# Kernel tuning notes

Hardware: AMD Instinct MI355X
Metric: run time of the kernel (lower is better)

Reference implementation:

```python
import jax, jax.numpy as jnp
import numpy as np
from jax import lax

D = 386      # model dim
H = 8        # heads
DH = 64      # dim per head
FF = 4 * D   # 1544, ff inner dim
FUSED = H * DH + DH + DH + 2 * FF  # 3728 fused proj width
S = 200      # patch_len


def setup_inputs() -> dict:
    key = jax.random.key(0)
    ks = iter(jax.random.split(key, 64))
    nrm = lambda shape, s=0.02: jax.random.normal(next(ks), shape, jnp.float32) * s
    inp = {"input": jax.random.normal(next(ks), (4, 2 * S, 3, 40, 40), jnp.float32)}
    inp["conv_w"] = nrm((D, 3, 3, 3), 0.1)
    inp["conv_b"] = jnp.zeros((D,), jnp.float32)
    inp["cls_token"] = nrm((D,), 1.0)
    for pre in ("uni", "mm"):
        inp[f"{pre}_ln"] = jnp.ones((4, D), jnp.float32)
        inp[f"{pre}_fused"] = nrm((4, D, FUSED))
        inp[f"{pre}_attn_out"] = nrm((4, H * DH, D))
        inp[f"{pre}_ff_out"] = nrm((4, FF, D))
    inp["ca_ln"] = jnp.ones((4, D), jnp.float32)
    inp["ca_q"] = nrm((4, D, H * DH))
    inp["ca_kv"] = nrm((4, D, 2 * DH))
    inp["ca_out"] = nrm((4, H * DH, D))
    inp["ca_ff1"] = nrm((4, D, 2 * FF))
    inp["ca_ff2"] = nrm((4, FF, D))
    inp["logit_ln"] = jnp.ones((D,), jnp.float32)
    inp["logit_w"] = nrm((D, 2))
    return inp


def layer_norm(x, g, eps=1e-5):
    m = x.mean(-1, keepdims=True)
    v = ((x - m) ** 2).mean(-1, keepdims=True)
    return (x - m) * lax.rsqrt(v + eps) * g


def rotate_half(t):
    t1, t2 = jnp.split(t, 2, axis=-1)
    return jnp.concatenate([-t2, t1], axis=-1)


def rotary_pos(n, d):
    inv = 1.0 / (10000.0 ** (jnp.arange(0, d, 2, dtype=jnp.float32) / d))
    fr = jnp.arange(n, dtype=jnp.float32)[:, None] * inv[None, :]
    return jnp.concatenate([fr, fr], axis=-1)  # [n, d]


def ptb(x, g, wf, wo, wff):
    # ParallelTransformerBlock (no residual): multi-query attn + parallel SwiGLU ff
    b, n, _ = x.shape
    xn = layer_norm(x, g)
    f = xn @ wf  # [b,n,FUSED]
    q = f[..., : H * DH].reshape(b, n, H, DH).transpose(0, 2, 1, 3)  # [b,h,n,d]
    k = f[..., H * DH : H * DH + DH]          # [b,n,d] single-head
    v = f[..., H * DH + DH : H * DH + 2 * DH]  # [b,n,d]
    ff = f[..., H * DH + 2 * DH :]
    pos = rotary_pos(n, DH)
    c, s = jnp.cos(pos), jnp.sin(pos)
    q = q * c + rotate_half(q) * s
    k = k * c + rotate_half(k) * s
    q = q * (DH ** -0.5)
    sim = jnp.einsum('bhid,bjd->bhij', q, k)
    mask = jnp.triu(jnp.ones((n, n), bool), 1)
    sim = jnp.where(mask, -jnp.finfo(sim.dtype).max, sim)
    attn = jax.nn.softmax(sim, axis=-1)
    out = jnp.einsum('bhij,bjd->bhid', attn, v).transpose(0, 2, 1, 3).reshape(b, n, H * DH)
    x1, gate = jnp.split(ff, 2, axis=-1)
    return out @ wo + (jax.nn.silu(gate) * x1) @ wff


def cross_attn(x, ctx, g, wq, wkv, wo, wf1, wf2):
    # CrossAttention with parallel_ff=True (context not normed)
    b, n, _ = x.shape
    xn = layer_norm(x, g)
    q = (xn @ wq).reshape(b, n, H, DH).transpose(0, 2, 1, 3) * (DH ** -0.5)
    k, v = jnp.split(ctx @ wkv, 2, axis=-1)  # [b,m,d] each, single-head
    sim = jnp.einsum('bhid,bjd->bhij', q, k)
    attn = jax.nn.softmax(sim, axis=-1)
    out = jnp.einsum('bhij,bjd->bhid', attn, v).transpose(0, 2, 1, 3).reshape(b, n, H * DH) @ wo
    h1, gate = jnp.split(xn @ wf1, 2, axis=-1)
    return out + (jax.nn.silu(gate) * h1) @ wf2


def reference(input, conv_w, conv_b, cls_token, uni_ln, uni_fused, uni_attn_out, uni_ff_out,
              mm_ln, mm_fused, mm_attn_out, mm_ff_out, ca_ln, ca_q, ca_kv, ca_out,
              ca_ff1, ca_ff2, logit_ln, logit_w):
    b = input.shape[0]

    def embed(img):  # [b,S,3,40,40] -> [b,S+1,D]
        x = img.reshape(b * S, 3, 40, 40)
        x = lax.conv_general_dilated(x, conv_w, (2, 2), 'VALID',
                                     dimension_numbers=('NCHW', 'OIHW', 'NCHW'))
        x = jax.nn.relu(x + conv_b[None, :, None, None])
        x = x.mean(axis=(2, 3)).reshape(b, S, D)  # adaptive avg pool (1,1)
        cls = jnp.broadcast_to(cls_token, (b, 1, D))
        return jnp.concatenate([x, cls], axis=1)

    # original forward uses embed_abnormal for BOTH chunks
    a = embed(input[:, :S])
    nrm = embed(input[:, S:])
    for i in range(4):
        a = a + ptb(a, uni_ln[i], uni_fused[i], uni_attn_out[i], uni_ff_out[i])
        nrm = nrm + ptb(nrm, uni_ln[i], uni_fused[i], uni_attn_out[i], uni_ff_out[i])
    for i in range(4):
        a = a + ptb(a, mm_ln[i], mm_fused[i], mm_attn_out[i], mm_ff_out[i])
        a = a + cross_attn(a, nrm, ca_ln[i], ca_q[i], ca_kv[i], ca_out[i], ca_ff1[i], ca_ff2[i])
    cls = a[:, -1]
    return layer_norm(cls, logit_ln) @ logit_w
```

## Files before the change

kernel.cpp:

```cpp
#include <hip/hip_runtime.h>
#include <hip/hip_bf16.h>
#include <math.h>

#define Dm 386
#define Hh 8
#define DHd 64
#define FFf 1544
#define FUS 3728
#define STOK 200
#define NTOK 201

typedef __attribute__((ext_vector_type(8))) short bf16x8;
typedef __attribute__((ext_vector_type(4))) float f32x4;

__device__ inline void gload16(const void* g, void* lds) {
  __builtin_amdgcn_global_load_lds((const __attribute__((address_space(1))) void*)g,
                                   (__attribute__((address_space(3))) void*)lds, 16, 0, 0);
}

__device__ inline short bfb(float v) {
  union { float f; unsigned u; } c; c.f = v;
  unsigned r = (c.u + 0x7fff + ((c.u >> 16) & 1)) >> 16;
  if ((c.u & 0x7f800000) == 0x7f800000) r = c.u >> 16;
  return (short)r;
}

__device__ inline void stage_coords(int lane, int& sr, int& sg) {
  int o = lane * 16;
  int rhi = (o >> 7) & 7;
  int r2 = (o >> 8) & 1;
  int r0 = ((o >> 6) & 1) ^ r2;
  sr = (rhi << 1) | r0;
  sg = ((o >> 4) & 3) ^ (sr & 3);
}

__global__ void misc_prep_kernel(const float* __restrict__ cw, __hip_bfloat16* __restrict__ wt,
                                 float* __restrict__ ct, float* __restrict__ st,
                                 const float* __restrict__ cls, float* __restrict__ act) {
  int b = blockIdx.x, t = threadIdx.x;
  if (b < 50) {
    int idx = b * 256 + t;
    if (idx < 400 * 32) {
      int n = idx >> 5, k = idx & 31;
      float v = (n < Dm && k < 27) ? cw[n * 27 + k] : 0.f;
      wt[idx] = __float2bfloat16(v);
    }
  } else if (b < 76) {
    int idx = (b - 50) * 256 + t;
    if (idx < 208 * 32) {
      int i = idx >> 5, d = idx & 31;
      float inv = exp2f((float)d * -0.41524101186f);
      float a = (float)i * inv;
      ct[idx] = cosf(a);
      st[idx] = sinf(a);
    }
  } else {
    int idx = (b - 76) * 256 + t;
    if (idx < 8 * Dm) {
      int r = idx / Dm, d = idx - r * Dm;
      act[((size_t)r * NTOK + STOK) * Dm + d] = cls[d];
    }
  }
}

struct CvtPack {
  const float* W[11];
  __hip_bfloat16* Bt[11];
};

__device__ void convert_body(int id, float* tile, const CvtPack& p) {
  static const int KK[11]    = {386, 512, 1544, 386, 512, 1544, 386, 386, 512, 386, 1544};
  static const int NN[11]    = {3728, 386, 386, 3728, 386, 386, 512, 128, 386, 3088, 386};
  static const int KPO[11]   = {416, 512, 1568, 416, 512, 1568, 416, 416, 512, 416, 1568};
  static const int KPOUT[11] = {416, 2080, 2080, 416, 2080, 2080, 416, 416, 2080, 416, 2080};
  static const int NTIL[11]  = {30, 4, 4, 30, 4, 4, 4, 1, 4, 25, 4};
  static const int LSTR[11]  = {1597440, 1064960, 1064960, 1597440, 1064960, 1064960,
                                1544192, 53248, 1064960, 1544192, 1064960};
  static const int CNT[11]   = {840, 128, 400, 840, 128, 400, 112, 28, 128, 700, 400};
  int wi = 0;
  while (wi < 10 && id >= CNT[wi]) { id -= CNT[wi]; ++wi; }
  int K = KK[wi], N = NN[wi];
  int ntil = NTIL[wi];
  int kpout = KPOUT[wi];
  int z = id & 3; id >>= 2;
  int kt = id / ntil, bx = id - kt * ntil;
  int k0 = kt * 64, n0 = bx * 128;
  const float* Wl = p.W[wi] + (size_t)z * K * N;
  __hip_bfloat16* Btl = p.Bt[wi] + (size_t)z * LSTR[wi];

  int tid = threadIdx.x;
  bool nfull = (n0 + 128 <= N);

  if (nfull && (N & 3) == 0) {
    int t4 = tid & 31, tk = tid >> 5;
    int nb = n0 + t4 * 4;
    #pragma unroll
    for (int j = 0; j < 4; ++j) {
      int kl = tk + 16 * j;
      int k = k0 + kl;
      float4 v = {0.f, 0.f, 0.f, 0.f};
      if (k < K) v = *(const float4*)(Wl + (size_t)k * N + nb);
      float* tr = tile + kl * 130 + t4 * 4;
      tr[0] = v.x; tr[1] = v.y; tr[2] = v.z; tr[3] = v.w;
    }
  } else {
    int t2 = tid & 63, tk = tid >> 6;
    int nb = n0 + t2 * 2;
    #pragma unroll
    for (int j = 0; j < 8; ++j) {
      int kl = tk + 8 * j;
      int k = k0 + kl;
      float2 v = {0.f, 0.f};
      if (k < K) {
        const float* src = Wl + (size_t)k * N + nb;
        if (nfull) {
          v = *(const float2*)src;
        } else {
          if (nb < N) v.x = src[0];
          if (nb + 1 < N) v.y = src[1];
        }
      }
      tile[kl * 130 + t2 * 2] = v.x;
      tile[kl * 130 + t2 * 2 + 1] = v.y;
    }
  }
  __syncthreads();

  int kv = KPO[wi] - k0; if (kv > 64) kv = 64;
  int tk8 = tid & 7;
  int nr = tid >> 3;
  if (tk8 * 8 < kv) {
    #pragma unroll
    for (int h = 0; h < 2; ++h) {
      int n = nr + 64 * h;
      __hip_bfloat16 out[8] __attribute__((aligned(16)));
      #pragma unroll
      for (int e = 0; e < 8; ++e)
        out[e] = __float2bfloat16(tile[(tk8 * 8 + e) * 130 + n]);
      *(int4*)(Btl + (size_t)(n0 + n) * kpout + k0 + tk8 * 8) = *(const int4*)out;
    }
  }
}

__device__ void conv_body(int img, char* smem,
                          const float* __restrict__ input, const __hip_bfloat16* __restrict__ wt,
                          const float* __restrict__ conv_b, float* __restrict__ act) {
  __hip_bfloat16* patches = (__hip_bfloat16*)smem;
  float* pooled = (float*)smem;
  float* biasS = (float*)(smem + 29440);

  int bi = img / 400, fi = img % 400;
  int srow = (fi < STOK) ? bi : (4 + bi);
  int tok = (fi < STOK) ? fi : (fi - STOK);
  float* dst = act + ((size_t)srow * NTOK + tok) * Dm;

  int tid = threadIdx.x;
  const float* img_base = input + (size_t)img * 4800;
  for (int i = tid; i < 400; i += 512) biasS[i] = (i < Dm) ? -conv_b[i] : 0.f;

  for (int p = tid; p < 368; p += 512) {
    short rowv[32] __attribute__((aligned(16)));
    #pragma unroll
    for (int k = 27; k < 32; ++k) rowv[k] = 0;
    if (p < 361) {
      int oy = p / 19, ox = p - oy * 19;
      const float* bp = img_base + (2 * oy) * 40 + 2 * ox;
      #pragma unroll
      for (int c = 0; c < 3; ++c) {
        #pragma unroll
        for (int ky = 0; ky < 3; ++ky) {
          const float* rp = bp + c * 1600 + ky * 40;
          #pragma unroll
          for (int kx = 0; kx < 3; ++kx)
            rowv[c * 9 + ky * 3 + kx] = bfb(rp[kx]);
        }
      }
    } else {
      #pragma unroll
      for (int k = 0; k < 27; ++k) rowv[k] = 0;
    }
    int4* dv = (int4*)(patches + p * 40);
    const int4* sv = (const int4*)rowv;
    #pragma unroll
    for (int q = 0; q < 4; ++q) dv[q] = sv[q];
  }
  __syncthreads();

  int lane = tid & 63, w = tid >> 6;
  int col = lane & 15, rgrp = lane >> 4;

  bf16x8 af[3];
  #pragma unroll
  for (int t = 0; t < 3; ++t) {
    int m = w * 3 + t;
    int row = (m < 23) ? (m * 16 + col) : 0;
    af[t] = *(const bf16x8*)&patches[row * 40 + rgrp * 8];
  }
  __syncthreads();

  for (int n = 0; n < 25; ++n) {
    bf16x8 bfrag = *(const bf16x8*)&wt[(n * 16 + col) * 32 + rgrp * 8];
    float nb = biasS[n * 16 + col];
    f32x4 a0 = {0.f, 0.f, 0.f, 0.f}, a1 = {0.f, 0.f, 0.f, 0.f};
    a0 = __builtin_amdgcn_mfma_f32_16x16x32_bf16(af[0], bfrag, a0, 0, 0, 0);
    a1 = __builtin_amdgcn_mfma_f32_16x16x32_bf16(af[1], bfrag, a1, 0, 0, 0);
    float psum = 0.f;
    #pragma unroll
    for (int j = 0; j < 4; ++j) psum += fmaxf(a0[j], nb);
    if (w == 7) {
      #pragma unroll
      for (int j = 0; j < 4; ++j) {
        int rr = 352 + rgrp * 4 + j;
        psum += (rr < 361) ? fmaxf(a1[j], nb) : 0.f;
      }
    } else {
      #pragma unroll
      for (int j = 0; j < 4; ++j) psum += fmaxf(a1[j], nb);
      f32x4 a2 = {0.f, 0.f, 0.f, 0.f};
      a2 = __builtin_amdgcn_mfma_f32_16x16x32_bf16(af[2], bfrag, a2, 0, 0, 0);
      #pragma unroll
      for (int j = 0; j < 4; ++j) psum += fmaxf(a2[j], nb);
    }
    psum += __shfl_xor(psum, 16);
    psum += __shfl_xor(psum, 32);
    if (lane < 16) pooled[w * 400 + n * 16 + lane] = psum;
  }
  __syncthreads();
  for (int d = tid; d < Dm; d += 512) {
    float s = 0.f;
    #pragma unroll
    for (int ww = 0; ww < 8; ++ww) s += pooled[ww * 400 + d];
    dst[d] = s * (1.f / 361.f) + conv_b[d];
  }
}

__global__ __launch_bounds__(512) void prep_conv_kernel(
    CvtPack p, const float* __restrict__ input, const __hip_bfloat16* __restrict__ wt,
    const float* __restrict__ conv_b, float* __restrict__ act) {
  __shared__ __align__(16) char smem[33280];
  int bid = blockIdx.x;
  int g = bid / 18, r = bid - g * 18;
  if (r < 5) {
    conv_body(g * 5 + r, smem, input, wt, conv_b, act);
  } else {
    int cid = g * 13 + (r - 5);
    if (cid < 4104) convert_body(cid, (float*)smem, p);
  }
}

__global__ __launch_bounds__(64) void ln_kernel(const float* __restrict__ x,
                                                const float* __restrict__ g,
                                                __hip_bfloat16* __restrict__ y) {
  size_t row = blockIdx.x;
  const float* xr = x + row * Dm;
  __hip_bfloat16* yr = y + row * 416;
  int t = threadIdx.x;
  float v[7];
  float lsum = 0.f, lsq = 0.f;
  #pragma unroll
  for (int j = 0; j < 7; ++j) {
    int c = t + 64 * j;
    float val = (c < Dm) ? xr[c] : 0.f;
    v[j] = val;
    lsum += val;
    lsq += val * val;
  }
  #pragma unroll
  for (int o = 32; o > 0; o >>= 1) { lsum += __shfl_xor(lsum, o); lsq += __shfl_xor(lsq, o); }
  float mean = lsum * (1.f / 386.f);
  float var = lsq * (1.f / 386.f) - mean * mean;
  float inv = rsqrtf(var + 1e-5f);
  #pragma unroll
  for (int j = 0; j < 7; ++j) {
    int c = t + 64 * j;
    if (c < 416) {
      float out = (c < Dm) ? (v[j] - mean) * inv * g[c] : 0.f;
      yr[c] = __float2bfloat16(out);
    }
  }
}

template<bool ACC>
__global__ __launch_bounds__(256) void mfma_mm(
    const __hip_bfloat16* __restrict__ A, const __hip_bfloat16* __restrict__ Bt,
    float* __restrict__ C, int M, int N, int Kp) {
  __shared__ short As[128 * 32];
  __shared__ short Bs[128 * 32];
  int tid = threadIdx.x;
  int lane = tid & 63, w = tid >> 6;
  int wr = w >> 1, wc = w & 1;
  int bm = blockIdx.y * 128, bn = blockIdx.x * 128;
  f32x4 acc[4][4] = {};

  int sr, sg;
  stage_coords(lane, sr, sg);
  const __hip_bfloat16* Abase = A + (size_t)(bm + w * 16 + sr) * Kp + sg * 8;
  const __hip_bfloat16* Bbase = Bt + (size_t)(bn + w * 16 + sr) * Kp + sg * 8;
  short* AsW1 = As + w * 512;
  short* AsW2 = As + 2048 + w * 512;
  short* BsW1 = Bs + w * 512;
  short* BsW2 = Bs + 2048 + w * 512;
  size_t rstep = (size_t)64 * Kp;
  int key = (lane & 7) << 4;
  int kg16 = (lane >> 4) * 16;

  for (int k0 = 0; k0 < Kp; k0 += 32) {
    gload16(Abase + k0, AsW1);
    gload16(Abase + k0 + rstep, AsW2);
    gload16(Bbase + k0, BsW1);
    gload16(Bbase + k0 + rstep, BsW2);
    __syncthreads();
    bf16x8 af[4], bfr[4];
    #pragma unroll
    for (int m = 0; m < 4; ++m) {
      int R = wr * 64 + m * 16 + (lane & 15);
      af[m] = *(const bf16x8*)((const char*)As + ((R * 64 + kg16) ^ key));
    }
    #pragma unroll
    for (int n = 0; n < 4; ++n) {
      int R = wc * 64 + n * 16 + (lane & 15);
      bfr[n] = *(const bf16x8*)((const char*)Bs + ((R * 64 + kg16) ^ key));
    }
    #pragma unroll
    for (int m = 0; m < 4; ++m)
      #pragma unroll
      for (int n = 0; n < 4; ++n)
        acc[m][n] = __builtin_amdgcn_mfma_f32_16x16x32_bf16(af[m], bfr[n], acc[m][n], 0, 0, 0);
    __syncthreads();
  }

  int col = lane & 15, rbase = (lane >> 4) * 4;
  #pragma unroll
  for (int m = 0; m < 4; ++m) {
    #pragma unroll
    for (int n = 0; n < 4; ++n) {
      #pragma unroll
      for (int j = 0; j < 4; ++j) {
        int gr = bm + wr * 64 + m * 16 + rbase + j;
        int gc = bn + wc * 64 + n * 16 + col;
        if (gr < M && gc < N) {
          size_t idx = (size_t)gr * N + gc;
          if (ACC) C[idx] += acc[m][n][j]; else C[idx] = acc[m][n][j];
        }
      }
    }
  }
}

__global__ __launch_bounds__(256) void mfma_mm64(
    const __hip_bfloat16* __restrict__ A, const __hip_bfloat16* __restrict__ Bt,
    float* __restrict__ C, int M, int N, int Kp) {
  __shared__ short As[64 * 32];
  __shared__ short Bs[64 * 32];
  int tid = threadIdx.x;
  int lane = tid & 63, w = tid >> 6;
  int wr = w >> 1, wc = w & 1;
  int bm = blockIdx.y * 64, bn = blockIdx.x * 64;
  f32x4 acc[2][2] = {};

  int sr, sg;
  stage_coords(lane, sr, sg);
  const __hip_bfloat16* Abase = A + (size_t)(bm + w * 16 + sr) * Kp + sg * 8;
  const __hip_bfloat16* Bbase = Bt + (size_t)(bn + w * 16 + sr) * Kp + sg * 8;
  short* AsW = As + w * 512;
  short* BsW = Bs + w * 512;
  int key = (lane & 7) << 4;
  int kg16 = (lane >> 4) * 16;

  for (int k0 = 0; k0 < Kp; k0 += 32) {
    gload16(Abase + k0, AsW);
    gload16(Bbase + k0, BsW);
    __syncthreads();
    bf16x8 af[2], bfr[2];
    #pragma unroll
    for (int m = 0; m < 2; ++m) {
      int R = wr * 32 + m * 16 + (lane & 15);
      af[m] = *(const bf16x8*)((const char*)As + ((R * 64 + kg16) ^ key));
    }
    #pragma unroll
    for (int n = 0; n < 2; ++n) {
      int R = wc * 32 + n * 16 + (lane & 15);
      bfr[n] = *(const bf16x8*)((const char*)Bs + ((R * 64 + kg16) ^ key));
    }
    #pragma unroll
    for (int m = 0; m < 2; ++m)
      #pragma unroll
      for (int n = 0; n < 2; ++n)
        acc[m][n] = __builtin_amdgcn_mfma_f32_16x16x32_bf16(af[m], bfr[n], acc[m][n], 0, 0, 0);
    __syncthreads();
  }

  int col = lane & 15, rbase = (lane >> 4) * 4;
  #pragma unroll
  for (int m = 0; m < 2; ++m) {
    #pragma unroll
    for (int n = 0; n < 2; ++n) {
      #pragma unroll
      for (int j = 0; j < 4; ++j) {
        int gr = bm + wr * 32 + m * 16 + rbase + j;
        int gc = bn + wc * 32 + n * 16 + col;
        if (gr < M && gc < N) C[(size_t)gr * N + gc] = acc[m][n][j];
      }
    }
  }
}

__global__ __launch_bounds__(256) void mfma_mm64a(
    const __hip_bfloat16* __restrict__ A, const __hip_bfloat16* __restrict__ Bt,
    float* __restrict__ C, int M, int N, int Kp, int chunk) {
  int kbeg = blockIdx.z * chunk;
  if (kbeg >= Kp) return;
  int kend = min(Kp, kbeg + chunk);
  __shared__ short As[64 * 32];
  __shared__ short Bs[64 * 32];
  int tid = threadIdx.x;
  int lane = tid & 63, w = tid >> 6;
  int wr = w >> 1, wc = w & 1;
  int bm = blockIdx.y * 64, bn = blockIdx.x * 64;
  f32x4 acc[2][2] = {};

  int sr, sg;
  stage_coords(lane, sr, sg);
  const __hip_bfloat16* Abase = A + (size_t)(bm + w * 16 + sr) * Kp + sg * 8;
  const __hip_bfloat16* Bbase = Bt + (size_t)(bn + w * 16 + sr) * Kp + sg * 8;
  short* AsW = As + w * 512;
  short* BsW = Bs + w * 512;
  int key = (lane & 7) << 4;
  int kg16 = (lane >> 4) * 16;

  for (int k0 = kbeg; k0 < kend; k0 += 32) {
    gload16(Abase + k0, AsW);
    gload16(Bbase + k0, BsW);
    __syncthreads();
    bf16x8 af[2], bfr[2];
    #pragma unroll
    for (int m = 0; m < 2; ++m) {
      int R = wr * 32 + m * 16 + (lane & 15);
      af[m] = *(const bf16x8*)((const char*)As + ((R * 64 + kg16) ^ key));
    }
    #pragma unroll
    for (int n = 0; n < 2; ++n) {
      int R = wc * 32 + n * 16 + (lane & 15);
      bfr[n] = *(const bf16x8*)((const char*)Bs + ((R * 64 + kg16) ^ key));
    }
    #pragma unroll
    for (int m = 0; m < 2; ++m)
      #pragma unroll
      for (int n = 0; n < 2; ++n)
        acc[m][n] = __builtin_amdgcn_mfma_f32_16x16x32_bf16(af[m], bfr[n], acc[m][n], 0, 0, 0);
    __syncthreads();
  }

  int col = lane & 15, rbase = (lane >> 4) * 4;
  #pragma unroll
  for (int m = 0; m < 2; ++m) {
    #pragma unroll
    for (int n = 0; n < 2; ++n) {
      #pragma unroll
      for (int j = 0; j < 4; ++j) {
        int gr = bm + wr * 32 + m * 16 + rbase + j;
        int gc = bn + wc * 32 + n * 16 + col;
        if (gr < M && gc < N) unsafeAtomicAdd(&C[(size_t)gr * N + gc], acc[m][n][j]);
      }
    }
  }
}

__global__ void convert_a_kernel(const float* __restrict__ src, __hip_bfloat16* __restrict__ dst,
                                 int M, int K, int Kp) {
  int chunks = Kp >> 3;
  int idx = blockIdx.x * blockDim.x + threadIdx.x;
  if (idx >= M * chunks) return;
  int r = idx / chunks, ch = idx - r * chunks;
  int c = ch * 8;
  const float* sr = src + (size_t)r * K;
  __hip_bfloat16 out[8] __attribute__((aligned(16)));
  #pragma unroll
  for (int e = 0; e < 8; e += 2) {
    int cc = c + e;
    float2 v = {0.f, 0.f};
    if (cc + 1 < K) v = *(const float2*)(sr + cc);
    else if (cc < K) v.x = sr[cc];
    out[e] = __float2bfloat16(v.x);
    out[e + 1] = __float2bfloat16(v.y);
  }
  *(int4*)(dst + (size_t)r * Kp + c) = *(const int4*)out;
}

__global__ __launch_bounds__(256) void attn_silu_kernel(
    const float* __restrict__ Q, int qstride,
    const float* __restrict__ K, int kstride,
    const float* __restrict__ V, int vstride,
    __hip_bfloat16* __restrict__ O, int ostride,
    int causal, float scale,
    const float* __restrict__ ct, const float* __restrict__ st, int dorope,
    int nb, int rows, int x1off, int gateoff) {
  int nf = 26 * nb;
  int tid = threadIdx.x;

  if ((int)blockIdx.x >= nf) {
    int idx = ((int)blockIdx.x - nf) * 256 + tid;
    if (idx >= rows * 196) return;
    int r = idx / 196, ch = idx - r * 196;
    int c = ch * 8;
    __hip_bfloat16 out[8] __attribute__((aligned(16)));
    if (c < FFf) {
      const float* sr = Q + (size_t)r * qstride;
      float4 xa = *(const float4*)(sr + x1off + c);
      float4 xb = *(const float4*)(sr + x1off + c + 4);
      float4 ga = *(const float4*)(sr + gateoff + c);
      float4 gb = *(const float4*)(sr + gateoff + c + 4);
      float xv[8] = {xa.x, xa.y, xa.z, xa.w, xb.x, xb.y, xb.z, xb.w};
      float gv[8] = {ga.x, ga.y, ga.z, ga.w, gb.x, gb.y, gb.z, gb.w};
      #pragma unroll
      for (int e = 0; e < 8; ++e) {
        float g = gv[e];
        out[e] = __float2bfloat16(g / (1.f + __expf(-g)) * xv[e]);
      }
    } else {
      #pragma unroll
      for (int e = 0; e < 8; ++e) out[e] = __float2bfloat16(0.f);
    }
    *(int4*)(O + 512 + (size_t)r * ostride + c) = *(const int4*)out;
    return;
  }

  __shared__ __align__(16) char smembuf[59392];
  short* Ks  = (short*)smembuf;
  short* Ps  = (short*)smembuf;
  short* VTs = (short*)(smembuf + 29696);

  int bb = blockIdx.x / 26;
  int i0 = (blockIdx.x % 26) * 8;
  int lane = tid & 63, w = tid >> 6;
  const float* Qb = Q + (size_t)bb * NTOK * qstride;
  const float* Kb = K + (size_t)bb * NTOK * kstride;
  const float* Vb = V + (size_t)bb * NTOK * vstride;

  int ntiles = causal ? min(13, (i0 + 7) / 16 + 1) : 13;
  int jstage = ntiles * 16;
  int jm = min(jstage, 201);

  {
    int4 z = {0, 0, 0, 0};
    int4* vt4 = (int4*)VTs;
    for (int idx = tid; idx < 64 * 232 * 2 / 16; idx += 256) vt4[idx] = z;
  }
  __syncthreads();

  for (int jj = tid >> 2; jj < jstage; jj += 64) {
    int q4 = tid & 3;
    int dbase = q4 * 16;
    const float* kro = Kb + (size_t)jj * kstride;
    float selfv[16], partv[16];
    #pragma unroll
    for (int f = 0; f < 4; ++f) {
      float4 kv = {0.f, 0.f, 0.f, 0.f};
      if (jj < 201) kv = ((const float4*)(kro + dbase))[f];
      selfv[f * 4 + 0] = kv.x; selfv[f * 4 + 1] = kv.y;
      selfv[f * 4 + 2] = kv.z; selfv[f * 4 + 3] = kv.w;
    }
    if (dorope && jj < 201) {
      int pbase = dbase ^ 32;
      #pragma unroll
      for (int f = 0; f < 4; ++f) {
        float4 kv = ((const float4*)(kro + pbase))[f];
        partv[f * 4 + 0] = kv.x; partv[f * 4 + 1] = kv.y;
        partv[f * 4 + 2] = kv.z; partv[f * 4 + 3] = kv.w;
      }
      const float* cr = ct + jj * 32 + (dbase & 31);
      const float* sr2 = st + jj * 32 + (dbase & 31);
      #pragma unroll
      for (int e = 0; e < 16; ++e) {
        float c = cr[e], s = sr2[e];
        selfv[e] = (dbase < 32) ? (selfv[e] * c - partv[e] * s)
                                : (selfv[e] * c + partv[e] * s);
      }
    }
    #pragma unroll
    for (int f = 0; f < 4; ++f) {
      short4 b;
      b.x = bfb(selfv[f * 4 + 0]); b.y = bfb(selfv[f * 4 + 1]);
      b.z = bfb(selfv[f * 4 + 2]); b.w = bfb(selfv[f * 4 + 3]);
      int colb = dbase * 2 + f * 8;
      *(short4*)((char*)Ks + (jj * 128 + (colb ^ ((jj & 7) << 4)))) = b;
    }
  }
  for (int jj = tid >> 3; jj < jm; jj += 32) {
    int e8 = (tid & 7) * 8;
    const float4* vr = (const float4*)(Vb + (size_t)jj * vstride + e8);
    float4 v0 = vr[0], v1 = vr[1];
    float vv[8] = {v0.x, v0.y, v0.z, v0.w, v1.x, v1.y, v1.z, v1.w};
    #pragma unroll
    for (int e = 0; e < 8; ++e) VTs[(e8 + e) * 232 + jj] = bfb(vv[e]);
  }

  int r = lane & 15, kg = lane >> 4;
  int rg = w * 16 + r;
  int iq = i0 + (rg >> 3);
  if (iq > 200) iq = 200;
  int h = rg & 7;
  const float* qr = Qb + (size_t)iq * qstride + h * 64 + kg * 8;
  float x1[8], x2[8];
  {
    float4 a0 = ((const float4*)qr)[0];
    float4 a1 = ((const float4*)(qr + 4))[0];
    float4 b0 = ((const float4*)(qr + 32))[0];
    float4 b1 = ((const float4*)(qr + 36))[0];
    x1[0] = a0.x; x1[1] = a0.y; x1[2] = a0.z; x1[3] = a0.w;
    x1[4] = a1.x; x1[5] = a1.y; x1[6] = a1.z; x1[7] = a1.w;
    x2[0] = b0.x; x2[1] = b0.y; x2[2] = b0.z; x2[3] = b0.w;
    x2[4] = b1.x; x2[5] = b1.y; x2[6] = b1.z; x2[7] = b1.w;
  }
  if (dorope) {
    const float* cr = ct + iq * 32 + kg * 8;
    const float* sr2 = st + iq * 32 + kg * 8;
    #pragma unroll
    for (int e = 0; e < 8; ++e) {
      float c = cr[e], s = sr2[e];
      float n1 = x1[e] * c - x2[e] * s;
      float n2 = x2[e] * c + x1[e] * s;
      x1[e] = n1; x2[e] = n2;
    }
  }
  bf16x8 aq[2];
  #pragma unroll
  for (int e = 0; e < 8; ++e) {
    aq[0][e] = bfb(x1[e] * scale);
    aq[1][e] = bfb(x2[e] * scale);
  }
  __syncthreads();

  int key = (lane & 7) << 4;
  f32x4 s[13];
  #pragma unroll
  for (int nt = 0; nt < 13; ++nt) {
    s[nt] = (f32x4){0.f, 0.f, 0.f, 0.f};
    if (nt < ntiles) {
      #pragma unroll
      for (int kt = 0; kt < 2; ++kt) {
        int row = nt * 16 + r;
        bf16x8 bk = *(const bf16x8*)((const char*)Ks + ((row * 128 + kt * 64 + kg * 16) ^ key));
        s[nt] = __builtin_amdgcn_mfma_f32_16x16x32_bf16(aq[kt], bk, s[nt], 0, 0, 0);
      }
    }
  }

  int jcol = lane & 15;
  int ibase[4];
  #pragma unroll
  for (int reg = 0; reg < 4; ++reg) ibase[reg] = i0 + ((w * 16 + kg * 4 + reg) >> 3);

  f32x4 mx = {-1e30f, -1e30f, -1e30f, -1e30f};
  #pragma unroll
  for (int nt = 0; nt < 13; ++nt) {
    if (nt >= ntiles) continue;
    int j = nt * 16 + jcol;
    #pragma unroll
    for (int reg = 0; reg < 4; ++reg) {
      bool ok = (j <= 200) && (!causal || j <= ibase[reg]);
      float sv = ok ? s[nt][reg] : -1e30f;
      s[nt][reg] = sv;
      mx[reg] = fmaxf(mx[reg], sv);
    }
  }
  #pragma unroll
  for (int o = 1; o < 16; o <<= 1) {
    #pragma unroll
    for (int reg = 0; reg < 4; ++reg) mx[reg] = fmaxf(mx[reg], __shfl_xor(mx[reg], o));
  }
  f32x4 sm = {0.f, 0.f, 0.f, 0.f};
  #pragma unroll
  for (int nt = 0; nt < 13; ++nt) {
    if (nt >= ntiles) continue;
    #pragma unroll
    for (int reg = 0; reg < 4; ++reg) {
      float p = __expf(s[nt][reg] - mx[reg]);
      s[nt][reg] = p;
      sm[reg] += p;
    }
  }
  #pragma unroll
  for (int o = 1; o < 16; o <<= 1) {
    #pragma unroll
    for (int reg = 0; reg < 4; ++reg) sm[reg] += __shfl_xor(sm[reg], o);
  }
  f32x4 inv;
  #pragma unroll
  for (int reg = 0; reg < 4; ++reg) inv[reg] = 1.f / sm[reg];

  __syncthreads();

  short* Pw = Ps + w * 16 * 232;
  #pragma unroll
  for (int nt = 0; nt < 13; ++nt) {
    #pragma unroll
    for (int reg = 0; reg < 4; ++reg) {
      float p = (nt < ntiles) ? s[nt][reg] * inv[reg] : 0.f;
      Pw[(kg * 4 + reg) * 232 + nt * 16 + jcol] = bfb(p);
    }
  }
  #pragma unroll
  for (int e = 0; e < 4; ++e) Pw[r * 232 + 208 + kg * 4 + e] = 0;

  int ktn = (jstage + 31) >> 5;
  f32x4 o[4] = {};
  #pragma unroll
  for (int kt = 0; kt < 7; ++kt) {
    if (kt >= ktn) continue;
    bf16x8 ap = *(const bf16x8*)((const char*)Pw + (r * 464 + kt * 64 + kg * 16));
    #pragma unroll
    for (int nt = 0; nt < 4; ++nt) {
      bf16x8 bv = *(const bf16x8*)((const char*)VTs + ((nt * 16 + r) * 464 + kt * 64 + kg * 16));
      o[nt] = __builtin_amdgcn_mfma_f32_16x16x32_bf16(ap, bv, o[nt], 0, 0, 0);
    }
  }

  #pragma unroll
  for (int nt = 0; nt < 4; ++nt) {
    #pragma unroll
    for (int reg = 0; reg < 4; ++reg) {
      int rc = w * 16 + kg * 4 + reg;
      int i = i0 + (rc >> 3);
      if (i < NTOK) {
        int hh = rc & 7;
        O[((size_t)bb * NTOK + i) * ostride + hh * 64 + nt * 16 + jcol] = __float2bfloat16(o[nt][reg]);
      }
    }
  }
}

__global__ __launch_bounds__(64) void head_kernel(const float* __restrict__ act,
                                                  const float* __restrict__ g,
                                                  const float* __restrict__ w,
                                                  float* __restrict__ out) {
  int bb = blockIdx.x;
  const float* xr = act + ((size_t)bb * NTOK + STOK) * Dm;
  int t = threadIdx.x;
  float v[7];
  float lsum = 0.f, lsq = 0.f;
  #pragma unroll
  for (int j = 0; j < 7; ++j) {
    int c = t + 64 * j;
    float val = (c < Dm) ? xr[c] : 0.f;
    v[j] = val;
    lsum += val;
    lsq += val * val;
  }
  #pragma unroll
  for (int o = 32; o > 0; o >>= 1) { lsum += __shfl_xor(lsum, o); lsq += __shfl_xor(lsq, o); }
  float mean = lsum * (1.f / 386.f);
  float var = lsq * (1.f / 386.f) - mean * mean;
  float inv = rsqrtf(var + 1e-5f);
  float d0 = 0.f, d1 = 0.f;
  #pragma unroll
  for (int j = 0; j < 7; ++j) {
    int c = t + 64 * j;
    if (c < Dm) {
      float xn = (v[j] - mean) * inv * g[c];
      d0 = fmaf(xn, w[2 * c], d0);
      d1 = fmaf(xn, w[2 * c + 1], d1);
    }
  }
  #pragma unroll
  for (int o = 32; o > 0; o >>= 1) { d0 += __shfl_xor(d0, o); d1 += __shfl_xor(d1, o); }
  if (t == 0) { out[2 * bb] = d0; out[2 * bb + 1] = d1; }
}

extern "C" void kernel_launch(void* const* d_in, const int* in_sizes, int n_in,
                              void* d_out, int out_size, void* d_ws, size_t ws_size,
                              hipStream_t stream) {
  const float* input     = (const float*)d_in[0];
  const float* conv_w    = (const float*)d_in[1];
  const float* conv_b    = (const float*)d_in[2];
  const float* cls_tok   = (const float*)d_in[3];
  const float* uni_ln    = (const float*)d_in[4];
  const float* uni_fused = (const float*)d_in[5];
  const float* uni_wo    = (const float*)d_in[6];
  const float* uni_wff   = (const float*)d_in[7];
  const float* mm_ln     = (const float*)d_in[8];
  const float* mm_fused  = (const float*)d_in[9];
  const float* mm_wo     = (const float*)d_in[10];
  const float* mm_wff    = (const float*)d_in[11];
  const float* ca_ln     = (const float*)d_in[12];
  const float* ca_q      = (const float*)d_in[13];
  const float* ca_kv     = (const float*)d_in[14];
  const float* ca_o      = (const float*)d_in[15];
  const float* ca_ff1    = (const float*)d_in[16];
  const float* ca_ff2    = (const float*)d_in[17];
  const float* logit_ln  = (const float*)d_in[18];
  const float* logit_w   = (const float*)d_in[19];
  (void)in_sizes; (void)n_in; (void)out_size; (void)ws_size;

  char* wsb = (char*)d_ws;
  size_t off = 0;
  auto alloc = [&](size_t bytes) { void* p = wsb + off; off += (bytes + 255) & ~(size_t)255; return p; };

  float* act   = (float*)alloc((size_t)8 * NTOK * Dm * 4);
  float* fbuf  = (float*)alloc((size_t)8 * NTOK * FUS * 4);
  float* kvall = (float*)alloc((size_t)4 * NTOK * 512 * 4);
  float* ctab  = (float*)alloc((size_t)208 * 32 * 4);
  float* stab  = (float*)alloc((size_t)208 * 32 * 4);
  __hip_bfloat16* xnb   = (__hip_bfloat16*)alloc((size_t)1664 * 416 * 2);
  __hip_bfloat16* ahbuf = (__hip_bfloat16*)alloc((size_t)1664 * 2080 * 2);
  __hip_bfloat16* ctxb  = (__hip_bfloat16*)alloc((size_t)896 * 416 * 2);
  __hip_bfloat16* cwT   = (__hip_bfloat16*)alloc((size_t)400 * 32 * 2);

  size_t sF  = (size_t)3840 * 416;
  size_t sOW = (size_t)512 * 2080;
  size_t sQF = (size_t)3712 * 416;
  __hip_bfloat16* uF  = (__hip_bfloat16*)alloc(4 * sF * 2);
  __hip_bfloat16* uOW = (__hip_bfloat16*)alloc(4 * sOW * 2);
  __hip_bfloat16* mF  = (__hip_bfloat16*)alloc(4 * sF * 2);
  __hip_bfloat16* mOW = (__hip_bfloat16*)alloc(4 * sOW * 2);
  __hip_bfloat16* cQF = (__hip_bfloat16*)alloc(4 * sQF * 2);
  __hip_bfloat16* cKV = (__hip_bfloat16*)alloc((size_t)512 * 416 * 2);
  __hip_bfloat16* cOF = (__hip_bfloat16*)alloc(4 * sOW * 2);

  CvtPack pk;
  pk.W[0] = uni_fused; pk.Bt[0] = uF;
  pk.W[1] = uni_wo;    pk.Bt[1] = uOW;
  pk.W[2] = uni_wff;   pk.Bt[2] = uOW + 512;
  pk.W[3] = mm_fused;  pk.Bt[3] = mF;
  pk.W[4] = mm_wo;     pk.Bt[4] = mOW;
  pk.W[5] = mm_wff;    pk.Bt[5] = mOW + 512;
  pk.W[6] = ca_q;      pk.Bt[6] = cQF;
  pk.W[7] = ca_kv;     pk.Bt[7] = cKV;
  pk.W[8] = ca_o;      pk.Bt[8] = cOF;
  pk.W[9] = ca_ff1;    pk.Bt[9] = cQF + (size_t)512 * 416;
  pk.W[10] = ca_ff2;   pk.Bt[10] = cOF + 512;

  misc_prep_kernel<<<89, 256, 0, stream>>>(conv_w, cwT, ctab, stab, cls_tok, act);
  prep_conv_kernel<<<5760, 512, 0, stream>>>(pk, input, cwT, conv_b, act);

  auto mmW = [&](const __hip_bfloat16* A, const __hip_bfloat16* Bt, float* C,
                 int M, int N, int Kp) {
    if (N <= 512) {
      dim3 g((N + 63) / 64, (M + 63) / 64);
      mfma_mm64<<<g, 256, 0, stream>>>(A, Bt, C, M, N, Kp);
    } else {
      dim3 g((N + 127) / 128, (M + 127) / 128);
      mfma_mm<false><<<g, 256, 0, stream>>>(A, Bt, C, M, N, Kp);
    }
  };
  auto mmA = [&](const __hip_bfloat16* A, const __hip_bfloat16* Bt, float* C,
                 int M, int N, int Kp) {
    int gx = (N + 63) / 64, gy = (M + 63) / 64;
    int blocks = gx * gy;
    int ksteps = Kp / 32;
    int nz = (blocks >= 512) ? 1 : (512 + blocks - 1) / blocks;
    if (nz > ksteps) nz = ksteps;
    int chunk = ((ksteps + nz - 1) / nz) * 32;
    dim3 g(gx, gy, nz);
    mfma_mm64a<<<g, 256, 0, stream>>>(A, Bt, C, M, N, Kp, chunk);
  };

  auto run_ptb = [&](float* x, int nb, const float* g, const __hip_bfloat16* wfB,
                     const __hip_bfloat16* owB) {
    int M = nb * NTOK;
    ln_kernel<<<M, 64, 0, stream>>>(x, g, xnb);
    mmW(xnb, wfB, fbuf, M, FUS, 416);
    int nblk = 26 * nb + (M * 196 + 255) / 256;
    attn_silu_kernel<<<nblk, 256, 0, stream>>>(
        fbuf, FUS, fbuf + 512, FUS, fbuf + 576, FUS, ahbuf, 2080, 1, 0.125f,
        ctab, stab, 1, nb, M, 640, 2184);
    mmA(ahbuf, owB, x, M, Dm, 2080);
  };

  for (int i = 0; i < 4; ++i)
    run_ptb(act, 8, uni_ln + i * Dm, uF + i * sF, uOW + i * sOW);

  const float* ctx = act + (size_t)4 * NTOK * Dm;
  convert_a_kernel<<<(804 * 52 + 255) / 256, 256, 0, stream>>>(ctx, ctxb, 804, Dm, 416);
  mmW(ctxb, cKV, kvall, 804, 512, 416);

  for (int i = 0; i < 4; ++i) {
    run_ptb(act, 4, mm_ln + i * Dm, mF + i * sF, mOW + i * sOW);
    int M = 4 * NTOK;
    ln_kernel<<<M, 64, 0, stream>>>(act, ca_ln + i * Dm, xnb);
    mmW(xnb, cQF + i * sQF, fbuf, M, 3712, 416);
    int nblk = 26 * 4 + (M * 196 + 255) / 256;
    attn_silu_kernel<<<nblk, 256, 0, stream>>>(
        fbuf, 3712, kvall + i * 128, 512, kvall + i * 128 + 64, 512, ahbuf, 2080,
        0, 0.125f, ctab, stab, 0, 4, M, 512, 2056);
    mmA(ahbuf, cOF + i * sOW, act, M, Dm, 2080);
  }

  head_kernel<<<4, 64, 0, stream>>>(act, logit_ln, logit_w, (float*)d_out);
}
```

Baseline: 779.8 us.

## Fuse next-layer LayerNorm and context bf16 conversion into split-K GEMM epilogue

```diff
diff --git a/kernel.cpp b/kernel.cpp
--- a/kernel.cpp
+++ b/kernel.cpp
@@ -36,7 +36,8 @@
 
 __global__ void misc_prep_kernel(const float* __restrict__ cw, __hip_bfloat16* __restrict__ wt,
                                  float* __restrict__ ct, float* __restrict__ st,
-                                 const float* __restrict__ cls, float* __restrict__ act) {
+                                 const float* __restrict__ cls, float* __restrict__ act,
+                                 unsigned* __restrict__ cnt) {
   int b = blockIdx.x, t = threadIdx.x;
   if (b < 50) {
     int idx = b * 256 + t;
@@ -54,12 +55,14 @@
       ct[idx] = cosf(a);
       st[idx] = sinf(a);
     }
-  } else {
+  } else if (b < 89) {
     int idx = (b - 76) * 256 + t;
     if (idx < 8 * Dm) {
       int r = idx / Dm, d = idx - r * Dm;
       act[((size_t)r * NTOK + STOK) * Dm + d] = cls[d];
     }
+  } else {
+    if (t < 32) cnt[t] = 0;
   }
 }
 
@@ -407,9 +410,11 @@
 
 __global__ __launch_bounds__(256) void mfma_mm64a(
     const __hip_bfloat16* __restrict__ A, const __hip_bfloat16* __restrict__ Bt,
-    float* __restrict__ C, int M, int N, int Kp, int chunk) {
+    float* __restrict__ C, int M, int N, int Kp, int chunk,
+    const float* __restrict__ gamma, __hip_bfloat16* __restrict__ lnout,
+    __hip_bfloat16* __restrict__ cvt_out, int cvtbeg,
+    unsigned* __restrict__ cnt, int ntotal) {
   int kbeg = blockIdx.z * chunk;
-  if (kbeg >= Kp) return;
   int kend = min(Kp, kbeg + chunk);
   __shared__ short As[64 * 32];
   __shared__ short Bs[64 * 32];
@@ -464,27 +469,59 @@
       }
     }
   }
-}
-
-__global__ void convert_a_kernel(const float* __restrict__ src, __hip_bfloat16* __restrict__ dst,
-                                 int M, int K, int Kp) {
-  int chunks = Kp >> 3;
-  int idx = blockIdx.x * blockDim.x + threadIdx.x;
-  if (idx >= M * chunks) return;
-  int r = idx / chunks, ch = idx - r * chunks;
-  int c = ch * 8;
-  const float* sr = src + (size_t)r * K;
-  __hip_bfloat16 out[8] __attribute__((aligned(16)));
-  #pragma unroll
-  for (int e = 0; e < 8; e += 2) {
-    int cc = c + e;
-    float2 v = {0.f, 0.f};
-    if (cc + 1 < K) v = *(const float2*)(sr + cc);
-    else if (cc < K) v.x = sr[cc];
-    out[e] = __float2bfloat16(v.x);
-    out[e + 1] = __float2bfloat16(v.y);
-  }
-  *(int4*)(dst + (size_t)r * Kp + c) = *(const int4*)out;
+
+  if (ntotal == 0) return;
+  __threadfence();
+  __syncthreads();
+  __shared__ int lastF;
+  if (tid == 0) {
+    unsigned prev = __hip_atomic_fetch_add(&cnt[blockIdx.y], 1u,
+                                           __ATOMIC_ACQ_REL, __HIP_MEMORY_SCOPE_AGENT);
+    lastF = (prev == (unsigned)(ntotal - 1));
+    if (lastF)
+      __hip_atomic_store(&cnt[blockIdx.y], 0u, __ATOMIC_RELAXED, __HIP_MEMORY_SCOPE_AGENT);
+  }
+  __syncthreads();
+  if (!lastF) return;
+
+  int rsel = tid >> 6;
+  for (int it = 0; it < 16; ++it) {
+    int row = bm + rsel * 16 + it;
+    if (row >= M) continue;
+    const float* xr = C + (size_t)row * N;
+    if (row < cvtbeg) {
+      float v[7];
+      float lsum = 0.f, lsq = 0.f;
+      #pragma unroll
+      for (int j = 0; j < 7; ++j) {
+        int c = lane + 64 * j;
+        float val = (c < Dm) ? xr[c] : 0.f;
+        v[j] = val;
+        lsum += val;
+        lsq += val * val;
+      }
+      #pragma unroll
+      for (int o = 32; o > 0; o >>= 1) { lsum += __shfl_xor(lsum, o); lsq += __shfl_xor(lsq, o); }
+      float mean = lsum * (1.f / 386.f);
+      float var = lsq * (1.f / 386.f) - mean * mean;
+      float inv = rsqrtf(var + 1e-5f);
+      #pragma unroll
+      for (int j = 0; j < 7; ++j) {
+        int c = lane + 64 * j;
+        if (c < 416)
+          lnout[(size_t)row * 416 + c] =
+              __float2bfloat16((c < Dm) ? (v[j] - mean) * inv * gamma[c] : 0.f);
+      }
+    } else {
+      #pragma unroll
+      for (int j = 0; j < 7; ++j) {
+        int c = lane + 64 * j;
+        if (c < 416)
+          cvt_out[(size_t)(row - cvtbeg) * 416 + c] =
+              __float2bfloat16((c < Dm) ? xr[c] : 0.f);
+      }
+    }
+  }
 }
 
 __global__ __launch_bounds__(256) void attn_silu_kernel(
@@ -801,6 +838,7 @@
   float* kvall = (float*)alloc((size_t)4 * NTOK * 512 * 4);
   float* ctab  = (float*)alloc((size_t)208 * 32 * 4);
   float* stab  = (float*)alloc((size_t)208 * 32 * 4);
+  unsigned* cnt = (unsigned*)alloc(128);
   __hip_bfloat16* xnb   = (__hip_bfloat16*)alloc((size_t)1664 * 416 * 2);
   __hip_bfloat16* ahbuf = (__hip_bfloat16*)alloc((size_t)1664 * 2080 * 2);
   __hip_bfloat16* ctxb  = (__hip_bfloat16*)alloc((size_t)896 * 416 * 2);
@@ -830,7 +868,7 @@
   pk.W[9] = ca_ff1;    pk.Bt[9] = cQF + (size_t)512 * 416;
   pk.W[10] = ca_ff2;   pk.Bt[10] = cOF + 512;
 
-  misc_prep_kernel<<<89, 256, 0, stream>>>(conv_w, cwT, ctab, stab, cls_tok, act);
+  misc_prep_kernel<<<90, 256, 0, stream>>>(conv_w, cwT, ctab, stab, cls_tok, act, cnt);
   prep_conv_kernel<<<5760, 512, 0, stream>>>(pk, input, cwT, conv_b, act);
 
   auto mmW = [&](const __hip_bfloat16* A, const __hip_bfloat16* Bt, float* C,
@@ -843,47 +881,60 @@
       mfma_mm<false><<<g, 256, 0, stream>>>(A, Bt, C, M, N, Kp);
     }
   };
-  auto mmA = [&](const __hip_bfloat16* A, const __hip_bfloat16* Bt, float* C,
-                 int M, int N, int Kp) {
+  auto mmAe = [&](const __hip_bfloat16* A, const __hip_bfloat16* Bt, float* C,
+                  int M, int N, int Kp,
+                  const float* gamma, __hip_bfloat16* lnout,
+                  __hip_bfloat16* cvt, int cvtbeg, bool ep) {
     int gx = (N + 63) / 64, gy = (M + 63) / 64;
     int blocks = gx * gy;
     int ksteps = Kp / 32;
     int nz = (blocks >= 512) ? 1 : (512 + blocks - 1) / blocks;
     if (nz > ksteps) nz = ksteps;
     int chunk = ((ksteps + nz - 1) / nz) * 32;
+    nz = (Kp + chunk - 1) / chunk;
+    int ntot = ep ? gx * nz : 0;
     dim3 g(gx, gy, nz);
-    mfma_mm64a<<<g, 256, 0, stream>>>(A, Bt, C, M, N, Kp, chunk);
+    mfma_mm64a<<<g, 256, 0, stream>>>(A, Bt, C, M, N, Kp, chunk,
+                                      gamma, lnout, cvt, cvtbeg, cnt, ntot);
   };
 
-  auto run_ptb = [&](float* x, int nb, const float* g, const __hip_bfloat16* wfB,
-                     const __hip_bfloat16* owB) {
-    int M = nb * NTOK;
-    ln_kernel<<<M, 64, 0, stream>>>(x, g, xnb);
-    mmW(xnb, wfB, fbuf, M, FUS, 416);
-    int nblk = 26 * nb + (M * 196 + 255) / 256;
+  ln_kernel<<<1608, 64, 0, stream>>>(act, uni_ln, xnb);
+  for (int i = 0; i < 4; ++i) {
+    int M = 8 * NTOK;
+    mmW(xnb, uF + i * sF, fbuf, M, FUS, 416);
+    int nblk = 26 * 8 + (M * 196 + 255) / 256;
     attn_silu_kernel<<<nblk, 256, 0, stream>>>(
         fbuf, FUS, fbuf + 512, FUS, fbuf + 576, FUS, ahbuf, 2080, 1, 0.125f,
-        ctab, stab, 1, nb, M, 640, 2184);
-    mmA(ahbuf, owB, x, M, Dm, 2080);
-  };
-
-  for (int i = 0; i < 4; ++i)
-    run_ptb(act, 8, uni_ln + i * Dm, uF + i * sF, uOW + i * sOW);
-
-  const float* ctx = act + (size_t)4 * NTOK * Dm;
-  convert_a_kernel<<<(804 * 52 + 255) / 256, 256, 0, stream>>>(ctx, ctxb, 804, Dm, 416);
+        ctab, stab, 1, 8, M, 640, 2184);
+    if (i < 3)
+      mmAe(ahbuf, uOW + i * sOW, act, M, Dm, 2080,
+           uni_ln + (i + 1) * Dm, xnb, nullptr, M, true);
+    else
+      mmAe(ahbuf, uOW + i * sOW, act, M, Dm, 2080,
+           mm_ln, xnb, ctxb, 804, true);
+  }
+
   mmW(ctxb, cKV, kvall, 804, 512, 416);
 
   for (int i = 0; i < 4; ++i) {
-    run_ptb(act, 4, mm_ln + i * Dm, mF + i * sF, mOW + i * sOW);
     int M = 4 * NTOK;
-    ln_kernel<<<M, 64, 0, stream>>>(act, ca_ln + i * Dm, xnb);
+    mmW(xnb, mF + i * sF, fbuf, M, FUS, 416);
+    int nblk = 26 * 4 + (M * 196 + 255) / 256;
+    attn_silu_kernel<<<nblk, 256, 0, stream>>>(
+        fbuf, FUS, fbuf + 512, FUS, fbuf + 576, FUS, ahbuf, 2080, 1, 0.125f,
+        ctab, stab, 1, 4, M, 640, 2184);
+    mmAe(ahbuf, mOW + i * sOW, act, M, Dm, 2080,
+         ca_ln + i * Dm, xnb, nullptr, M, true);
     mmW(xnb, cQF + i * sQF, fbuf, M, 3712, 416);
-    int nblk = 26 * 4 + (M * 196 + 255) / 256;
     attn_silu_kernel<<<nblk, 256, 0, stream>>>(
         fbuf, 3712, kvall + i * 128, 512, kvall + i * 128 + 64, 512, ahbuf, 2080,
         0, 0.125f, ctab, stab, 0, 4, M, 512, 2056);
-    mmA(ahbuf, cOF + i * sOW, act, M, Dm, 2080);
+    if (i < 3)
+      mmAe(ahbuf, cOF + i * sOW, act, M, Dm, 2080,
+           mm_ln + (i + 1) * Dm, xnb, nullptr, M, true);
+    else
+      mmAe(ahbuf, cOF + i * sOW, act, M, Dm, 2080,
+           nullptr, nullptr, nullptr, 0, false);
   }
 
   head_kernel<<<4, 64, 0, stream>>>(act, logit_ln, logit_w, (float*)d_out);
```

New measurement: 1.278 ms. 1.64x slower.

## Fuse K rotary and bf16 packing into fused-projection GEMM epilogue

Applied to the files above, without the earlier changes.

```diff
diff --git a/kernel.cpp b/kernel.cpp
--- a/kernel.cpp
+++ b/kernel.cpp
@@ -283,7 +283,9 @@
 template<bool ACC>
 __global__ __launch_bounds__(256) void mfma_mm(
     const __hip_bfloat16* __restrict__ A, const __hip_bfloat16* __restrict__ Bt,
-    float* __restrict__ C, int M, int N, int Kp) {
+    float* __restrict__ C, int M, int N, int Kp,
+    short* __restrict__ kout, short* __restrict__ vout,
+    const float* __restrict__ ct, const float* __restrict__ st, int kvtile) {
   __shared__ short As[128 * 32];
   __shared__ short Bs[128 * 32];
   int tid = threadIdx.x;
@@ -345,11 +347,40 @@
       }
     }
   }
-}
-
-__global__ __launch_bounds__(256) void mfma_mm64(
+
+  if ((int)blockIdx.x == kvtile) {
+    #pragma unroll
+    for (int m = 0; m < 4; ++m) {
+      #pragma unroll
+      for (int j = 0; j < 4; ++j) {
+        int gr = bm + wr * 64 + m * 16 + rbase + j;
+        if (gr >= M) continue;
+        int i = gr % NTOK;
+        if (wc == 0) {
+          #pragma unroll
+          for (int n = 0; n < 4; ++n) {
+            int d = n * 16 + col;
+            float cc = ct[i * 32 + (d & 31)];
+            float ss = st[i * 32 + (d & 31)];
+            float self = acc[m][n][j], part = acc[m][n ^ 2][j];
+            float outv = (d < 32) ? self * cc - part * ss : self * cc + part * ss;
+            kout[(size_t)gr * 64 + d] = bfb(outv);
+          }
+        } else {
+          #pragma unroll
+          for (int n = 0; n < 4; ++n) {
+            int d = n * 16 + col;
+            vout[(size_t)gr * 64 + d] = bfb(acc[m][n][j]);
+          }
+        }
+      }
+    }
+  }
+}
+
+__global__ __launch_bounds__(256) void mfma_mm64kv(
     const __hip_bfloat16* __restrict__ A, const __hip_bfloat16* __restrict__ Bt,
-    float* __restrict__ C, int M, int N, int Kp) {
+    short* __restrict__ kvb, int M, int Kp) {
   __shared__ short As[64 * 32];
   __shared__ short Bs[64 * 32];
   int tid = threadIdx.x;
@@ -391,6 +422,7 @@
   }
 
   int col = lane & 15, rbase = (lane >> 4) * 4;
+  int tx = blockIdx.x, layer = tx >> 1, half = tx & 1;
   #pragma unroll
   for (int m = 0; m < 2; ++m) {
     #pragma unroll
@@ -398,8 +430,9 @@
       #pragma unroll
       for (int j = 0; j < 4; ++j) {
         int gr = bm + wr * 32 + m * 16 + rbase + j;
-        int gc = bn + wc * 32 + n * 16 + col;
-        if (gr < M && gc < N) C[(size_t)gr * N + gc] = acc[m][n][j];
+        int d = wc * 32 + n * 16 + col;
+        if (gr < M)
+          kvb[((size_t)layer * 804 + gr) * 128 + half * 64 + d] = bfb(acc[m][n][j]);
       }
     }
   }
@@ -489,8 +522,8 @@
 
 __global__ __launch_bounds__(256) void attn_silu_kernel(
     const float* __restrict__ Q, int qstride,
-    const float* __restrict__ K, int kstride,
-    const float* __restrict__ V, int vstride,
+    const short* __restrict__ K, int kstride,
+    const short* __restrict__ V, int vstride,
     __hip_bfloat16* __restrict__ O, int ostride,
     int causal, float scale,
     const float* __restrict__ ct, const float* __restrict__ st, int dorope,
@@ -534,8 +567,8 @@
   int i0 = (blockIdx.x % 26) * 8;
   int lane = tid & 63, w = tid >> 6;
   const float* Qb = Q + (size_t)bb * NTOK * qstride;
-  const float* Kb = K + (size_t)bb * NTOK * kstride;
-  const float* Vb = V + (size_t)bb * NTOK * vstride;
+  const short* Kb = K + (size_t)bb * NTOK * kstride;
+  const short* Vb = V + (size_t)bb * NTOK * vstride;
 
   int ntiles = causal ? min(13, (i0 + 7) / 16 + 1) : 13;
   int jstage = ntiles * 16;
@@ -550,49 +583,27 @@
 
   for (int jj = tid >> 2; jj < jstage; jj += 64) {
     int q4 = tid & 3;
-    int dbase = q4 * 16;
-    const float* kro = Kb + (size_t)jj * kstride;
-    float selfv[16], partv[16];
+    short vk[16] __attribute__((aligned(16)));
+    if (jj < 201) {
+      const int4* kr = (const int4*)(Kb + (size_t)jj * kstride + q4 * 16);
+      ((int4*)vk)[0] = kr[0];
+      ((int4*)vk)[1] = kr[1];
+    } else {
+      #pragma unroll
+      for (int e = 0; e < 16; ++e) vk[e] = 0;
+    }
     #pragma unroll
     for (int f = 0; f < 4; ++f) {
-      float4 kv = {0.f, 0.f, 0.f, 0.f};
-      if (jj < 201) kv = ((const float4*)(kro + dbase))[f];
-      selfv[f * 4 + 0] = kv.x; selfv[f * 4 + 1] = kv.y;
-      selfv[f * 4 + 2] = kv.z; selfv[f * 4 + 3] = kv.w;
-    }
-    if (dorope && jj < 201) {
-      int pbase = dbase ^ 32;
-      #pragma unroll
-      for (int f = 0; f < 4; ++f) {
-        float4 kv = ((const float4*)(kro + pbase))[f];
-        partv[f * 4 + 0] = kv.x; partv[f * 4 + 1] = kv.y;
-        partv[f * 4 + 2] = kv.z; partv[f * 4 + 3] = kv.w;
-      }
-      const float* cr = ct + jj * 32 + (dbase & 31);
-      const float* sr2 = st + jj * 32 + (dbase & 31);
-      #pragma unroll
-      for (int e = 0; e < 16; ++e) {
-        float c = cr[e], s = sr2[e];
-        selfv[e] = (dbase < 32) ? (selfv[e] * c - partv[e] * s)
-                                : (selfv[e] * c + partv[e] * s);
-      }
-    }
-    #pragma unroll
-    for (int f = 0; f < 4; ++f) {
-      short4 b;
-      b.x = bfb(selfv[f * 4 + 0]); b.y = bfb(selfv[f * 4 + 1]);
-      b.z = bfb(selfv[f * 4 + 2]); b.w = bfb(selfv[f * 4 + 3]);
-      int colb = dbase * 2 + f * 8;
-      *(short4*)((char*)Ks + (jj * 128 + (colb ^ ((jj & 7) << 4)))) = b;
+      int colb = q4 * 32 + f * 8;
+      *(short4*)((char*)Ks + (jj * 128 + (colb ^ ((jj & 7) << 4)))) = *(short4*)&vk[f * 4];
     }
   }
   for (int jj = tid >> 3; jj < jm; jj += 32) {
     int e8 = (tid & 7) * 8;
-    const float4* vr = (const float4*)(Vb + (size_t)jj * vstride + e8);
-    float4 v0 = vr[0], v1 = vr[1];
-    float vv[8] = {v0.x, v0.y, v0.z, v0.w, v1.x, v1.y, v1.z, v1.w};
-    #pragma unroll
-    for (int e = 0; e < 8; ++e) VTs[(e8 + e) * 232 + jj] = bfb(vv[e]);
+    short vv[8] __attribute__((aligned(16)));
+    *(int4*)vv = *(const int4*)(Vb + (size_t)jj * vstride + e8);
+    #pragma unroll
+    for (int e = 0; e < 8; ++e) VTs[(e8 + e) * 232 + jj] = vv[e];
   }
 
   int r = lane & 15, kg = lane >> 4;
@@ -798,9 +809,11 @@
 
   float* act   = (float*)alloc((size_t)8 * NTOK * Dm * 4);
   float* fbuf  = (float*)alloc((size_t)8 * NTOK * FUS * 4);
-  float* kvall = (float*)alloc((size_t)4 * NTOK * 512 * 4);
   float* ctab  = (float*)alloc((size_t)208 * 32 * 4);
   float* stab  = (float*)alloc((size_t)208 * 32 * 4);
+  short* kbuf  = (short*)alloc((size_t)1608 * 64 * 2);
+  short* vbuf  = (short*)alloc((size_t)1608 * 64 * 2);
+  short* ckvb  = (short*)alloc((size_t)4 * 804 * 128 * 2);
   __hip_bfloat16* xnb   = (__hip_bfloat16*)alloc((size_t)1664 * 416 * 2);
   __hip_bfloat16* ahbuf = (__hip_bfloat16*)alloc((size_t)1664 * 2080 * 2);
   __hip_bfloat16* ctxb  = (__hip_bfloat16*)alloc((size_t)896 * 416 * 2);
@@ -833,15 +846,11 @@
   misc_prep_kernel<<<89, 256, 0, stream>>>(conv_w, cwT, ctab, stab, cls_tok, act);
   prep_conv_kernel<<<5760, 512, 0, stream>>>(pk, input, cwT, conv_b, act);
 
-  auto mmW = [&](const __hip_bfloat16* A, const __hip_bfloat16* Bt, float* C,
-                 int M, int N, int Kp) {
-    if (N <= 512) {
-      dim3 g((N + 63) / 64, (M + 63) / 64);
-      mfma_mm64<<<g, 256, 0, stream>>>(A, Bt, C, M, N, Kp);
-    } else {
-      dim3 g((N + 127) / 128, (M + 127) / 128);
-      mfma_mm<false><<<g, 256, 0, stream>>>(A, Bt, C, M, N, Kp);
-    }
+  auto mmWf = [&](const __hip_bfloat16* A, const __hip_bfloat16* Bt, float* C,
+                  int M, int N, int Kp, int kvtile) {
+    dim3 g((N + 127) / 128, (M + 127) / 128);
+    mfma_mm<false><<<g, 256, 0, stream>>>(A, Bt, C, M, N, Kp,
+                                          kbuf, vbuf, ctab, stab, kvtile);
   };
   auto mmA = [&](const __hip_bfloat16* A, const __hip_bfloat16* Bt, float* C,
                  int M, int N, int Kp) {
@@ -859,10 +868,10 @@
                      const __hip_bfloat16* owB) {
     int M = nb * NTOK;
     ln_kernel<<<M, 64, 0, stream>>>(x, g, xnb);
-    mmW(xnb, wfB, fbuf, M, FUS, 416);
+    mmWf(xnb, wfB, fbuf, M, FUS, 416, 4);
     int nblk = 26 * nb + (M * 196 + 255) / 256;
     attn_silu_kernel<<<nblk, 256, 0, stream>>>(
-        fbuf, FUS, fbuf + 512, FUS, fbuf + 576, FUS, ahbuf, 2080, 1, 0.125f,
+        fbuf, FUS, kbuf, 64, vbuf, 64, ahbuf, 2080, 1, 0.125f,
         ctab, stab, 1, nb, M, 640, 2184);
     mmA(ahbuf, owB, x, M, Dm, 2080);
   };
@@ -872,16 +881,20 @@
 
   const float* ctx = act + (size_t)4 * NTOK * Dm;
   convert_a_kernel<<<(804 * 52 + 255) / 256, 256, 0, stream>>>(ctx, ctxb, 804, Dm, 416);
-  mmW(ctxb, cKV, kvall, 804, 512, 416);
+  {
+    dim3 g(8, 13);
+    mfma_mm64kv<<<g, 256, 0, stream>>>(ctxb, cKV, ckvb, 804, 416);
+  }
 
   for (int i = 0; i < 4; ++i) {
     run_ptb(act, 4, mm_ln + i * Dm, mF + i * sF, mOW + i * sOW);
     int M = 4 * NTOK;
     ln_kernel<<<M, 64, 0, stream>>>(act, ca_ln + i * Dm, xnb);
-    mmW(xnb, cQF + i * sQF, fbuf, M, 3712, 416);
+    mmWf(xnb, cQF + i * sQF, fbuf, M, 3712, 416, -1);
     int nblk = 26 * 4 + (M * 196 + 255) / 256;
     attn_silu_kernel<<<nblk, 256, 0, stream>>>(
-        fbuf, 3712, kvall + i * 128, 512, kvall + i * 128 + 64, 512, ahbuf, 2080,
+        fbuf, 3712, ckvb + (size_t)i * 804 * 128, 128,
+        ckvb + (size_t)i * 804 * 128 + 64, 128, ahbuf, 2080,
         0, 0.125f, ctab, stab, 0, 4, M, 512, 2056);
     mmA(ahbuf, cOF + i * sOW, act, M, Dm, 2080);
   }
```

Result: no change. 790.7 us (+1.4%).
